# Kernel optimization log

Hardware: AMD Instinct MI355X
Metric: run time of the kernel (lower is better)

The kernel has to match this reference:

```python
import jax, jax.numpy as jnp
import numpy as np

N_NODES = 50000
E_RAW = 1600000
EMB_DIM = 32
HID = 128
OUT = 128


def setup_inputs() -> dict:
    key = jax.random.key(0)
    k1, k2, k3, k4, k5, k6 = jax.random.split(key, 6)
    x = jnp.arange(N_NODES, dtype=jnp.int64)
    edge_index = jax.random.randint(k1, (2, E_RAW), 0, N_NODES, dtype=jnp.int64)
    emb = jax.random.normal(k2, (N_NODES, EMB_DIM), dtype=jnp.float32)
    W1 = jax.random.normal(k3, (EMB_DIM, HID), dtype=jnp.float32) / np.sqrt(EMB_DIM)
    b1 = jnp.zeros((HID,), dtype=jnp.float32)
    W2 = jax.random.normal(k4, (HID, OUT), dtype=jnp.float32) / np.sqrt(HID)
    b2 = jnp.zeros((OUT,), dtype=jnp.float32)
    return {"x": x, "edge_index": edge_index, "emb": emb,
            "W1": W1, "b1": b1, "W2": W2, "b2": b2}


def _gcn_norm(edge_index, num_nodes):
    # add self-loops, then symmetric normalization deg^-1/2 A_hat deg^-1/2
    loop = jnp.arange(num_nodes, dtype=edge_index.dtype)
    src = jnp.concatenate([edge_index[0], loop])
    dst = jnp.concatenate([edge_index[1], loop])
    ones = jnp.ones(src.shape[0], dtype=jnp.float32)
    deg = jax.ops.segment_sum(ones, dst, num_segments=num_nodes)
    dinv = jax.lax.rsqrt(deg)  # deg >= 1 due to self-loops
    norm = dinv[src] * dinv[dst]  # [E+N]
    return src, dst, norm


def _gcn_conv(h, src, dst, norm, W, b, num_nodes):
    h = h @ W                                  # [N, d_out] dense GEMM
    msg = h[src] * norm[:, None]               # gather + edge scale
    agg = jax.ops.segment_sum(msg, dst, num_segments=num_nodes)  # scatter-add
    return agg + b


def reference(x, edge_index, emb, W1, b1, W2, b2):
    num_nodes = emb.shape[0]
    h = emb[x]                                 # embedding lookup
    src, dst, norm = _gcn_norm(edge_index, num_nodes)
    h = _gcn_conv(h, src, dst, norm, W1, b1, num_nodes)
    h = jax.nn.relu(h)
    out = _gcn_conv(h, src, dst, norm, W2, b2, num_nodes)
    return out
```

## Files before the change

### kernel.cpp

```cpp
#include <hip/hip_runtime.h>


#define NPP   6250
#define NC    32

static inline int cdiv(int a, int b){ return (a + b - 1) / b; }

__device__ __forceinline__ unsigned short f2bf(float f){
    unsigned int u = __float_as_uint(f);
    u += 0x7fffu + ((u >> 16) & 1u);
    return (unsigned short)(u >> 16);
}
__device__ __forceinline__ float bf2f(unsigned short b){
    return __uint_as_float(((unsigned int)b) << 16);
}

__global__ void k_zero_i32(int* __restrict__ p, int n){
    int i = blockIdx.x * blockDim.x + threadIdx.x;
    if (i < n) p[i] = 0;
}

__global__ __launch_bounds__(256) void k_bucket(const int* __restrict__ src,
        const int* __restrict__ dst, int E, int* __restrict__ staged,
        int* __restrict__ gcur, int npp, int C){
    __shared__ int qcnt[8];
    __shared__ int qbase[8];
    __shared__ int qbuf[8 * 256];
    int tid = threadIdx.x;
    if (tid < 8) qcnt[tid] = 0;
    __syncthreads();
    int e0 = blockIdx.x * 1024 + tid * 4;
    if (e0 + 3 < E){
        int4 d4 = *(const int4*)(dst + e0);
        int4 s4 = *(const int4*)(src + e0);
        int dd[4] = {d4.x, d4.y, d4.z, d4.w};
        int ss[4] = {s4.x, s4.y, s4.z, s4.w};
        #pragma unroll
        for (int i = 0; i < 4; i++){
            int p = dd[i] / npp;
            int pk = ((dd[i] - p * npp) << 17) | ss[i];
            int pos = atomicAdd(&qcnt[p], 1);
            if (pos < 256) qbuf[p * 256 + pos] = pk;
            else {
                int gp = atomicAdd(&gcur[p], 1);
                staged[(size_t)p * C + gp] = pk;
            }
        }
    } else {
        for (int e = e0; e < E && e < e0 + 4; e++){
            int d = dst[e], s = src[e];
            int p = d / npp;
            int pk = ((d - p * npp) << 17) | s;
            int pos = atomicAdd(&qcnt[p], 1);
            if (pos < 256) qbuf[p * 256 + pos] = pk;
            else {
                int gp = atomicAdd(&gcur[p], 1);
                staged[(size_t)p * C + gp] = pk;
            }
        }
    }
    __syncthreads();
    if (tid < 8){
        int nq = min(qcnt[tid], 256);
        qbase[tid] = (nq > 0) ? atomicAdd(&gcur[tid], nq) : 0;
    }
    __syncthreads();
    for (int b = 0; b < 8; b++){
        int nq = min(qcnt[b], 256);
        int gb = qbase[b];
        for (int i = tid; i < nq; i += 256)
            staged[(size_t)b * C + gb + i] = qbuf[b * 256 + i];
    }
}

__global__ __launch_bounds__(256) void k_hist(const int* __restrict__ staged,
        const int* __restrict__ gcur, int C, int CH, int npp, int* __restrict__ H){
    __shared__ int hist[NPP];
    int part  = blockIdx.x & 7;
    int chunk = blockIdx.x >> 3;
    int tid = threadIdx.x;
    for (int i = tid; i < npp; i += 256) hist[i] = 0;
    __syncthreads();
    int pc = gcur[part];
    int e0 = chunk * CH, e1 = min(e0 + CH, pc);
    const int* sd = staged + (size_t)part * C;
    for (int e = e0 + tid; e < e1; e += 256)
        atomicAdd(&hist[(unsigned)sd[e] >> 17], 1);
    __syncthreads();
    int* Hrow = H + (size_t)(part * NC + chunk) * npp;
    for (int i = tid; i < npp; i += 256) Hrow[i] = hist[i];
}

__global__ __launch_bounds__(256) void k_nodescan(int* __restrict__ H, int npp, int n,
        int* __restrict__ ecount, float* __restrict__ dinv, int* __restrict__ bsum){
    __shared__ int s[256];
    int t = blockIdx.x * 256 + threadIdx.x;
    int run = 0;
    if (t < 8 * npp && t < n){
        int p  = t / npp;
        int dl = t - p * npp;
        #pragma unroll
        for (int c = 0; c < NC; c++){
            size_t idx = (size_t)(p * NC + c) * npp + dl;
            int v = H[idx];
            H[idx] = run;
            run += v;
        }
        ecount[t] = run;
        dinv[t] = rsqrtf((float)run + 1.0f);
    }
    s[threadIdx.x] = run;
    __syncthreads();
    for (int d = 128; d > 0; d >>= 1){
        if (threadIdx.x < d) s[threadIdx.x] += s[threadIdx.x + d];
        __syncthreads();
    }
    if (threadIdx.x == 0) bsum[blockIdx.x] = s[0];
}

__global__ __launch_bounds__(256) void k_scanBC(const int* __restrict__ ecount, int n,
        const int* __restrict__ bsum, int nb, int* __restrict__ offsets){
    __shared__ int bs[256];
    __shared__ int s[256];
    int t = threadIdx.x;
    bs[t] = (t < nb) ? bsum[t] : 0;
    __syncthreads();
    if (t == 0){
        int run = 0;
        for (int b = 0; b < nb; b++){ int v = bs[b]; bs[b] = run; run += v; }
    }
    __syncthreads();
    int i = blockIdx.x * 256 + t;
    int v = (i < n) ? ecount[i] : 0;
    s[t] = v;
    __syncthreads();
    for (int d = 1; d < 256; d <<= 1){
        int x = (t >= d) ? s[t - d] : 0;
        __syncthreads();
        s[t] += x;
        __syncthreads();
    }
    if (i < n) offsets[i] = bs[blockIdx.x] + s[t] - v;
}

__global__ __launch_bounds__(256) void k_fill3(const int* __restrict__ staged,
        const int* __restrict__ gcur, int C, int CH, int npp,
        const int* __restrict__ H, const int* __restrict__ offsets,
        int* __restrict__ csr_src){
    __shared__ int cur[NPP];
    int part  = blockIdx.x & 7;
    int chunk = blockIdx.x >> 3;
    int tid = threadIdx.x;
    const int* Hrow = H + (size_t)(part * NC + chunk) * npp;
    for (int i = tid; i < npp; i += 256) cur[i] = Hrow[i];
    __syncthreads();
    int pc = gcur[part];
    int lo = part * npp;
    int e0 = chunk * CH, e1 = min(e0 + CH, pc);
    const int* sd = staged + (size_t)part * C;
    for (int e = e0 + tid; e < e1; e += 256){
        int pk = sd[e];
        int dl = (unsigned)pk >> 17;
        int r = atomicAdd(&cur[dl], 1);
        csr_src[offsets[lo + dl] + r] = pk & 0x1FFFF;
    }
}

__global__ void k_scale(const float* __restrict__ emb, const int* __restrict__ x,
                        const float* __restrict__ dinv, unsigned short* __restrict__ es, int n){
    int idx = blockIdx.x * blockDim.x + threadIdx.x;
    if (idx >= n * 32) return;
    int i = idx >> 5;
    int c = idx & 31;
    es[idx] = f2bf(emb[(size_t)x[i] * 32 + c] * dinv[i]);
}

__global__ __launch_bounds__(256) void k_l1(const unsigned short* __restrict__ es,
        const int* __restrict__ offsets, const int* __restrict__ ecount,
        const int* __restrict__ csr, const float* __restrict__ dinv,
        const float* __restrict__ W1, const float* __restrict__ b1,
        unsigned short* __restrict__ hs, int n){
    __shared__ float w[32 * 128];
    __shared__ float a1t[8][32];
    for (int i = threadIdx.x; i < 32 * 128; i += 256) w[i] = W1[i];
    int g    = threadIdx.x >> 5;
    int lane = threadIdx.x & 31;
    int node = blockIdx.x * 8 + g;
    if (node < n){
        int off = offsets[node], cnt = ecount[node];
        float s0 = bf2f(es[(size_t)node * 32 + lane]);
        float s1 = 0.f;
        int e = 0;
        for (; e + 8 <= cnt; e += 8){
            int i0 = csr[off + e + 0], i1 = csr[off + e + 1];
            int i2 = csr[off + e + 2], i3 = csr[off + e + 3];
            int i4 = csr[off + e + 4], i5 = csr[off + e + 5];
            int i6 = csr[off + e + 6], i7 = csr[off + e + 7];
            unsigned short v0 = es[(size_t)i0 * 32 + lane];
            unsigned short v1 = es[(size_t)i1 * 32 + lane];
            unsigned short v2 = es[(size_t)i2 * 32 + lane];
            unsigned short v3 = es[(size_t)i3 * 32 + lane];
            unsigned short v4 = es[(size_t)i4 * 32 + lane];
            unsigned short v5 = es[(size_t)i5 * 32 + lane];
            unsigned short v6 = es[(size_t)i6 * 32 + lane];
            unsigned short v7 = es[(size_t)i7 * 32 + lane];
            s0 += bf2f(v0) + bf2f(v2) + bf2f(v4) + bf2f(v6);
            s1 += bf2f(v1) + bf2f(v3) + bf2f(v5) + bf2f(v7);
        }
        for (; e < cnt; e++) s0 += bf2f(es[(size_t)csr[off + e] * 32 + lane]);
        a1t[g][lane] = dinv[node] * (s0 + s1);
    }
    __syncthreads();
    if (node >= n) return;
    int c4 = lane * 4;
    float4 acc = *(const float4*)(b1 + c4);
    #pragma unroll
    for (int k4 = 0; k4 < 8; k4++){
        float4 av = *(const float4*)&a1t[g][k4 * 4];
        float4 w0 = *(const float4*)&w[(k4 * 4 + 0) * 128 + c4];
        float4 w1 = *(const float4*)&w[(k4 * 4 + 1) * 128 + c4];
        float4 w2 = *(const float4*)&w[(k4 * 4 + 2) * 128 + c4];
        float4 w3 = *(const float4*)&w[(k4 * 4 + 3) * 128 + c4];
        acc.x += av.x * w0.x + av.y * w1.x + av.z * w2.x + av.w * w3.x;
        acc.y += av.x * w0.y + av.y * w1.y + av.z * w2.y + av.w * w3.y;
        acc.z += av.x * w0.z + av.y * w1.z + av.z * w2.z + av.w * w3.z;
        acc.w += av.x * w0.w + av.y * w1.w + av.z * w2.w + av.w * w3.w;
    }
    float dv = dinv[node];
    ushort4 o;
    o.x = f2bf(dv * fmaxf(acc.x, 0.f));
    o.y = f2bf(dv * fmaxf(acc.y, 0.f));
    o.z = f2bf(dv * fmaxf(acc.z, 0.f));
    o.w = f2bf(dv * fmaxf(acc.w, 0.f));
    *(ushort4*)(hs + (size_t)node * 128 + c4) = o;
}

__global__ __launch_bounds__(256) void k_l2(const unsigned short* __restrict__ hs,
        const int* __restrict__ offsets, const int* __restrict__ ecount,
        const int* __restrict__ csr, const float* __restrict__ dinv,
        const float* __restrict__ W2, const float* __restrict__ b2,
        float* __restrict__ out, int n){
    __shared__ float a2t[32 * 128];
    int g    = threadIdx.x >> 5;
    int lane = threadIdx.x & 31;
    int c4g  = lane * 4;
    #pragma unroll
    for (int j = 0; j < 4; j++){
        int nl = g + 8 * j;
        int node = blockIdx.x * 32 + nl;
        if (node < n){
            int off = offsets[node], cnt = ecount[node];
            ushort4 sv = *(const ushort4*)(hs + (size_t)node * 128 + c4g);
            float ax0 = bf2f(sv.x), ax1 = 0.f;
            float ay0 = bf2f(sv.y), ay1 = 0.f;
            float az0 = bf2f(sv.z), az1 = 0.f;
            float aw0 = bf2f(sv.w), aw1 = 0.f;
            int e = 0;
            for (; e + 8 <= cnt; e += 8){
                int i0 = csr[off + e + 0], i1 = csr[off + e + 1];
                int i2 = csr[off + e + 2], i3 = csr[off + e + 3];
                int i4 = csr[off + e + 4], i5 = csr[off + e + 5];
                int i6 = csr[off + e + 6], i7 = csr[off + e + 7];
                ushort4 v0 = *(const ushort4*)(hs + (size_t)i0 * 128 + c4g);
                ushort4 v1 = *(const ushort4*)(hs + (size_t)i1 * 128 + c4g);
                ushort4 v2 = *(const ushort4*)(hs + (size_t)i2 * 128 + c4g);
                ushort4 v3 = *(const ushort4*)(hs + (size_t)i3 * 128 + c4g);
                ushort4 v4 = *(const ushort4*)(hs + (size_t)i4 * 128 + c4g);
                ushort4 v5 = *(const ushort4*)(hs + (size_t)i5 * 128 + c4g);
                ushort4 v6 = *(const ushort4*)(hs + (size_t)i6 * 128 + c4g);
                ushort4 v7 = *(const ushort4*)(hs + (size_t)i7 * 128 + c4g);
                ax0 += bf2f(v0.x) + bf2f(v2.x) + bf2f(v4.x) + bf2f(v6.x);
                ax1 += bf2f(v1.x) + bf2f(v3.x) + bf2f(v5.x) + bf2f(v7.x);
                ay0 += bf2f(v0.y) + bf2f(v2.y) + bf2f(v4.y) + bf2f(v6.y);
                ay1 += bf2f(v1.y) + bf2f(v3.y) + bf2f(v5.y) + bf2f(v7.y);
                az0 += bf2f(v0.z) + bf2f(v2.z) + bf2f(v4.z) + bf2f(v6.z);
                az1 += bf2f(v1.z) + bf2f(v3.z) + bf2f(v5.z) + bf2f(v7.z);
                aw0 += bf2f(v0.w) + bf2f(v2.w) + bf2f(v4.w) + bf2f(v6.w);
                aw1 += bf2f(v1.w) + bf2f(v3.w) + bf2f(v5.w) + bf2f(v7.w);
            }
            for (; e < cnt; e++){
                ushort4 v = *(const ushort4*)(hs + (size_t)csr[off + e] * 128 + c4g);
                ax0 += bf2f(v.x); ay0 += bf2f(v.y); az0 += bf2f(v.z); aw0 += bf2f(v.w);
            }
            float dv = dinv[node];
            float4 r;
            r.x = dv * (ax0 + ax1); r.y = dv * (ay0 + ay1);
            r.z = dv * (az0 + az1); r.w = dv * (aw0 + aw1);
            *(float4*)&a2t[nl * 128 + c4g] = r;
        }
    }
    __syncthreads();
    int c4 = lane * 4;
    int r0 = (threadIdx.x >> 5) * 4;
    float4 bias = *(const float4*)(b2 + c4);
    float4 acc0 = bias, acc1 = bias, acc2 = bias, acc3 = bias;
    for (int k = 0; k < 128; k += 4){
        float4 a0  = *(const float4*)&a2t[(r0 + 0) * 128 + k];
        float4 a1v = *(const float4*)&a2t[(r0 + 1) * 128 + k];
        float4 a2v = *(const float4*)&a2t[(r0 + 2) * 128 + k];
        float4 a3v = *(const float4*)&a2t[(r0 + 3) * 128 + k];
        #pragma unroll
        for (int kk = 0; kk < 4; kk++){
            float4 wv = *(const float4*)(W2 + (size_t)(k + kk) * 128 + c4);
            float b0 = (kk == 0) ? a0.x  : (kk == 1) ? a0.y  : (kk == 2) ? a0.z  : a0.w;
            float b1v= (kk == 0) ? a1v.x : (kk == 1) ? a1v.y : (kk == 2) ? a1v.z : a1v.w;
            float b2v= (kk == 0) ? a2v.x : (kk == 1) ? a2v.y : (kk == 2) ? a2v.z : a2v.w;
            float b3 = (kk == 0) ? a3v.x : (kk == 1) ? a3v.y : (kk == 2) ? a3v.z : a3v.w;
            acc0.x += b0 * wv.x; acc0.y += b0 * wv.y; acc0.z += b0 * wv.z; acc0.w += b0 * wv.w;
            acc1.x += b1v * wv.x; acc1.y += b1v * wv.y; acc1.z += b1v * wv.z; acc1.w += b1v * wv.w;
            acc2.x += b2v * wv.x; acc2.y += b2v * wv.y; acc2.z += b2v * wv.z; acc2.w += b2v * wv.w;
            acc3.x += b3 * wv.x; acc3.y += b3 * wv.y; acc3.z += b3 * wv.z; acc3.w += b3 * wv.w;
        }
    }
    int rb = blockIdx.x * 32 + r0;
    if (rb + 0 < n) *(float4*)(out + (size_t)(rb + 0) * 128 + c4) = acc0;
    if (rb + 1 < n) *(float4*)(out + (size_t)(rb + 1) * 128 + c4) = acc1;
    if (rb + 2 < n) *(float4*)(out + (size_t)(rb + 2) * 128 + c4) = acc2;
    if (rb + 3 < n) *(float4*)(out + (size_t)(rb + 3) * 128 + c4) = acc3;
}

extern "C" void kernel_launch(void* const* d_in, const int* in_sizes, int n_in,
                              void* d_out, int out_size, void* d_ws, size_t ws_size,
                              hipStream_t stream){
    const int*   x    = (const int*)d_in[0];
    const int*   ei   = (const int*)d_in[1];
    const float* emb  = (const float*)d_in[2];
    const float* W1   = (const float*)d_in[3];
    const float* b1   = (const float*)d_in[4];
    const float* W2   = (const float*)d_in[5];
    const float* b2   = (const float*)d_in[6];
    const int N = in_sizes[0];
    const int E = in_sizes[1] / 2;
    const int* srcv = ei;
    const int* dstv = ei + E;
    float* out = (float*)d_out;

    char* p = (char*)d_ws;
    auto alloc = [&](size_t bytes) -> char* {
        char* r = p; p += (bytes + 255) & ~(size_t)255; return r;
    };
    int nb = cdiv(N, 256);
    int*            ecount  = (int*)           alloc((size_t)(N + 8) * 4);
    int*            gcur    = ecount + N;
    int*            offsets = (int*)           alloc((size_t)N * 4);
    int*            bsum    = (int*)           alloc((size_t)nb * 4);
    float*          dinv    = (float*)         alloc((size_t)N * 4);
    int*            csr     = (int*)           alloc((size_t)E * 4);
    unsigned short* es      = (unsigned short*)alloc((size_t)N * 32 * 2);
    int*            H       = (int*)           alloc((size_t)8 * NC * NPP * 4);
    unsigned short* hs      = (unsigned short*)alloc((size_t)N * 128 * 2);
    int*            staged  = (int*)           alloc((size_t)(E + 8 * 65536) * 4);
    (void)ws_size; (void)n_in; (void)out_size;

    const int npp = cdiv(N, 8);
    const int C   = E / 8 + 65536;
    const int CH  = cdiv(C, NC);

    k_zero_i32<<<1, 64, 0, stream>>>(gcur, 8);
    k_bucket  <<<cdiv(E, 1024), 256, 0, stream>>>(srcv, dstv, E, staged, gcur, npp, C);
    k_hist    <<<8 * NC, 256, 0, stream>>>(staged, gcur, C, CH, npp, H);
    k_nodescan<<<nb, 256, 0, stream>>>(H, npp, N, ecount, dinv, bsum);
    k_scanBC  <<<nb, 256, 0, stream>>>(ecount, N, bsum, nb, offsets);
    k_fill3   <<<8 * NC, 256, 0, stream>>>(staged, gcur, C, CH, npp, H, offsets, csr);

    k_scale <<<cdiv(N * 32, 256), 256, 0, stream>>>(emb, x, dinv, es, N);
    k_l1    <<<cdiv(N, 8), 256, 0, stream>>>(es, offsets, ecount, csr, dinv, W1, b1, hs, N);

    k_l2    <<<cdiv(N, 32), 256, 0, stream>>>(hs, offsets, ecount, csr, dinv, W2, b2, out, N);
}
```

Baseline: 269.8 us.

## Partition CSR neighbors by source-node quarter to localize layer-2 gathers

Result: slower. 352.7 us (+30.7%).

```diff
diff --git a/kernel.cpp b/kernel.cpp
--- a/kernel.cpp
+++ b/kernel.cpp
@@ -3,6 +3,11 @@
 
 #define NPP   6250
 #define NC    32
+#define CAP   96
+#define CAPP  97
+#define NPB   40
+
+typedef float vfloat4 __attribute__((ext_vector_type(4)));
 
 static inline int cdiv(int a, int b){ return (a + b - 1) / b; }
 
@@ -13,6 +18,11 @@
 }
 __device__ __forceinline__ float bf2f(unsigned short b){
     return __uint_as_float(((unsigned int)b) << 16);
+}
+
+__device__ __forceinline__ void nt_store4(float* p, const float4& v){
+    vfloat4 t = {v.x, v.y, v.z, v.w};
+    __builtin_nontemporal_store(t, (vfloat4*)p);
 }
 
 __global__ void k_zero_i32(int* __restrict__ p, int n){
@@ -164,6 +174,44 @@
         int r = atomicAdd(&cur[dl], 1);
         csr_src[offsets[lo + dl] + r] = pk & 0x1FFFF;
     }
+}
+
+__global__ __launch_bounds__(128) void k_part(const int* __restrict__ offsets,
+        const int* __restrict__ ecount, int* __restrict__ csr,
+        int4* __restrict__ bnd4, int n, int th1, int th2, int th3){
+    __shared__ int buf[128 * CAPP];
+    int t = threadIdx.x;
+    int node = blockIdx.x * 128 + t;
+    if (node >= n) return;
+    int off = offsets[node], cnt = ecount[node];
+    int4 b;
+    if (cnt <= CAP){
+        int* mb = buf + t * CAPP;
+        int c0 = 0, c1 = 0, c2 = 0;
+        for (int i = 0; i < cnt; i++){
+            int v = csr[off + i];
+            mb[i] = v;
+            c0 += (v < th1);
+            c1 += (v >= th1) & (v < th2);
+            c2 += (v >= th2) & (v < th3);
+        }
+        int p1 = c0, p2 = c0 + c1, p3 = c0 + c1 + c2;
+        int q0 = 0, q1 = p1, q2 = p2, q3 = p3;
+        for (int i = 0; i < cnt; i++){
+            int v = mb[i];
+            int pos;
+            if      (v < th1) pos = q0++;
+            else if (v < th2) pos = q1++;
+            else if (v < th3) pos = q2++;
+            else              pos = q3++;
+            csr[off + pos] = v;
+        }
+        b = make_int4(p1, p2, p3, cnt);
+    } else {
+        int q = cnt >> 2;
+        b = make_int4(q, 2 * q, 3 * q, cnt);
+    }
+    bnd4[node] = b;
 }
 
 __global__ void k_scale(const float* __restrict__ emb, const int* __restrict__ x,
@@ -235,32 +283,47 @@
     *(ushort4*)(hs + (size_t)node * 128 + c4) = o;
 }
 
-__global__ __launch_bounds__(256) void k_l2(const unsigned short* __restrict__ hs,
-        const int* __restrict__ offsets, const int* __restrict__ ecount,
+__global__ __launch_bounds__(256, 5) void k_l2(const unsigned short* __restrict__ hs,
+        const int* __restrict__ offsets, const int4* __restrict__ bnd4,
         const int* __restrict__ csr, const float* __restrict__ dinv,
         const float* __restrict__ W2, const float* __restrict__ b2,
         float* __restrict__ out, int n){
-    __shared__ float a2t[32 * 128];
+    __shared__ float a2t[NPB * 128];
     int g    = threadIdx.x >> 5;
     int lane = threadIdx.x & 31;
     int c4g  = lane * 4;
+    float4 acc[5];
     #pragma unroll
-    for (int j = 0; j < 4; j++){
-        int nl = g + 8 * j;
-        int node = blockIdx.x * 32 + nl;
+    for (int j = 0; j < 5; j++){
+        int node = blockIdx.x * NPB + g + 8 * j;
         if (node < n){
-            int off = offsets[node], cnt = ecount[node];
             ushort4 sv = *(const ushort4*)(hs + (size_t)node * 128 + c4g);
-            float ax0 = bf2f(sv.x), ax1 = 0.f;
-            float ay0 = bf2f(sv.y), ay1 = 0.f;
-            float az0 = bf2f(sv.z), az1 = 0.f;
-            float aw0 = bf2f(sv.w), aw1 = 0.f;
-            int e = 0;
-            for (; e + 8 <= cnt; e += 8){
-                int i0 = csr[off + e + 0], i1 = csr[off + e + 1];
-                int i2 = csr[off + e + 2], i3 = csr[off + e + 3];
-                int i4 = csr[off + e + 4], i5 = csr[off + e + 5];
-                int i6 = csr[off + e + 6], i7 = csr[off + e + 7];
+            acc[j].x = bf2f(sv.x); acc[j].y = bf2f(sv.y);
+            acc[j].z = bf2f(sv.z); acc[j].w = bf2f(sv.w);
+        } else {
+            acc[j].x = acc[j].y = acc[j].z = acc[j].w = 0.f;
+        }
+    }
+    #pragma unroll
+    for (int c = 0; c < 4; c++){
+        #pragma unroll
+        for (int j = 0; j < 5; j++){
+            int node = blockIdx.x * NPB + g + 8 * j;
+            if (node >= n) continue;
+            int off = offsets[node];
+            int4 b = bnd4[node];
+            int e0 = (c == 0) ? 0   : (c == 1) ? b.x : (c == 2) ? b.y : b.z;
+            int e1 = (c == 0) ? b.x : (c == 1) ? b.y : (c == 2) ? b.z : b.w;
+            int e = e0;
+            for (; e + 8 <= e1; e += 8){
+                int i0 = __builtin_nontemporal_load(csr + off + e + 0);
+                int i1 = __builtin_nontemporal_load(csr + off + e + 1);
+                int i2 = __builtin_nontemporal_load(csr + off + e + 2);
+                int i3 = __builtin_nontemporal_load(csr + off + e + 3);
+                int i4 = __builtin_nontemporal_load(csr + off + e + 4);
+                int i5 = __builtin_nontemporal_load(csr + off + e + 5);
+                int i6 = __builtin_nontemporal_load(csr + off + e + 6);
+                int i7 = __builtin_nontemporal_load(csr + off + e + 7);
                 ushort4 v0 = *(const ushort4*)(hs + (size_t)i0 * 128 + c4g);
                 ushort4 v1 = *(const ushort4*)(hs + (size_t)i1 * 128 + c4g);
                 ushort4 v2 = *(const ushort4*)(hs + (size_t)i2 * 128 + c4g);
@@ -269,36 +332,51 @@
                 ushort4 v5 = *(const ushort4*)(hs + (size_t)i5 * 128 + c4g);
                 ushort4 v6 = *(const ushort4*)(hs + (size_t)i6 * 128 + c4g);
                 ushort4 v7 = *(const ushort4*)(hs + (size_t)i7 * 128 + c4g);
-                ax0 += bf2f(v0.x) + bf2f(v2.x) + bf2f(v4.x) + bf2f(v6.x);
-                ax1 += bf2f(v1.x) + bf2f(v3.x) + bf2f(v5.x) + bf2f(v7.x);
-                ay0 += bf2f(v0.y) + bf2f(v2.y) + bf2f(v4.y) + bf2f(v6.y);
-                ay1 += bf2f(v1.y) + bf2f(v3.y) + bf2f(v5.y) + bf2f(v7.y);
-                az0 += bf2f(v0.z) + bf2f(v2.z) + bf2f(v4.z) + bf2f(v6.z);
-                az1 += bf2f(v1.z) + bf2f(v3.z) + bf2f(v5.z) + bf2f(v7.z);
-                aw0 += bf2f(v0.w) + bf2f(v2.w) + bf2f(v4.w) + bf2f(v6.w);
-                aw1 += bf2f(v1.w) + bf2f(v3.w) + bf2f(v5.w) + bf2f(v7.w);
+                acc[j].x += bf2f(v0.x) + bf2f(v1.x) + bf2f(v2.x) + bf2f(v3.x)
+                          + bf2f(v4.x) + bf2f(v5.x) + bf2f(v6.x) + bf2f(v7.x);
+                acc[j].y += bf2f(v0.y) + bf2f(v1.y) + bf2f(v2.y) + bf2f(v3.y)
+                          + bf2f(v4.y) + bf2f(v5.y) + bf2f(v6.y) + bf2f(v7.y);
+                acc[j].z += bf2f(v0.z) + bf2f(v1.z) + bf2f(v2.z) + bf2f(v3.z)
+                          + bf2f(v4.z) + bf2f(v5.z) + bf2f(v6.z) + bf2f(v7.z);
+                acc[j].w += bf2f(v0.w) + bf2f(v1.w) + bf2f(v2.w) + bf2f(v3.w)
+                          + bf2f(v4.w) + bf2f(v5.w) + bf2f(v6.w) + bf2f(v7.w);
             }
-            for (; e < cnt; e++){
-                ushort4 v = *(const ushort4*)(hs + (size_t)csr[off + e] * 128 + c4g);
-                ax0 += bf2f(v.x); ay0 += bf2f(v.y); az0 += bf2f(v.z); aw0 += bf2f(v.w);
+            if (e < e1){
+                #pragma unroll
+                for (int i = 0; i < 8; i++){
+                    int ei = min(e + i, e1 - 1);
+                    int idx = __builtin_nontemporal_load(csr + off + ei);
+                    ushort4 v = *(const ushort4*)(hs + (size_t)idx * 128 + c4g);
+                    if (e + i < e1){
+                        acc[j].x += bf2f(v.x); acc[j].y += bf2f(v.y);
+                        acc[j].z += bf2f(v.z); acc[j].w += bf2f(v.w);
+                    }
+                }
             }
+        }
+    }
+    #pragma unroll
+    for (int j = 0; j < 5; j++){
+        int node = blockIdx.x * NPB + g + 8 * j;
+        if (node < n){
             float dv = dinv[node];
             float4 r;
-            r.x = dv * (ax0 + ax1); r.y = dv * (ay0 + ay1);
-            r.z = dv * (az0 + az1); r.w = dv * (aw0 + aw1);
-            *(float4*)&a2t[nl * 128 + c4g] = r;
+            r.x = dv * acc[j].x; r.y = dv * acc[j].y;
+            r.z = dv * acc[j].z; r.w = dv * acc[j].w;
+            *(float4*)&a2t[(g + 8 * j) * 128 + c4g] = r;
         }
     }
     __syncthreads();
     int c4 = lane * 4;
-    int r0 = (threadIdx.x >> 5) * 4;
+    int r0 = g * 5;
     float4 bias = *(const float4*)(b2 + c4);
-    float4 acc0 = bias, acc1 = bias, acc2 = bias, acc3 = bias;
+    float4 o0 = bias, o1 = bias, o2 = bias, o3 = bias, o4 = bias;
     for (int k = 0; k < 128; k += 4){
-        float4 a0  = *(const float4*)&a2t[(r0 + 0) * 128 + k];
-        float4 a1v = *(const float4*)&a2t[(r0 + 1) * 128 + k];
-        float4 a2v = *(const float4*)&a2t[(r0 + 2) * 128 + k];
-        float4 a3v = *(const float4*)&a2t[(r0 + 3) * 128 + k];
+        float4 a0 = *(const float4*)&a2t[(r0 + 0) * 128 + k];
+        float4 a1v= *(const float4*)&a2t[(r0 + 1) * 128 + k];
+        float4 a2v= *(const float4*)&a2t[(r0 + 2) * 128 + k];
+        float4 a3v= *(const float4*)&a2t[(r0 + 3) * 128 + k];
+        float4 a4v= *(const float4*)&a2t[(r0 + 4) * 128 + k];
         #pragma unroll
         for (int kk = 0; kk < 4; kk++){
             float4 wv = *(const float4*)(W2 + (size_t)(k + kk) * 128 + c4);
@@ -306,17 +384,20 @@
             float b1v= (kk == 0) ? a1v.x : (kk == 1) ? a1v.y : (kk == 2) ? a1v.z : a1v.w;
             float b2v= (kk == 0) ? a2v.x : (kk == 1) ? a2v.y : (kk == 2) ? a2v.z : a2v.w;
             float b3 = (kk == 0) ? a3v.x : (kk == 1) ? a3v.y : (kk == 2) ? a3v.z : a3v.w;
-            acc0.x += b0 * wv.x; acc0.y += b0 * wv.y; acc0.z += b0 * wv.z; acc0.w += b0 * wv.w;
-            acc1.x += b1v * wv.x; acc1.y += b1v * wv.y; acc1.z += b1v * wv.z; acc1.w += b1v * wv.w;
-            acc2.x += b2v * wv.x; acc2.y += b2v * wv.y; acc2.z += b2v * wv.z; acc2.w += b2v * wv.w;
-            acc3.x += b3 * wv.x; acc3.y += b3 * wv.y; acc3.z += b3 * wv.z; acc3.w += b3 * wv.w;
-        }
-    }
-    int rb = blockIdx.x * 32 + r0;
-    if (rb + 0 < n) *(float4*)(out + (size_t)(rb + 0) * 128 + c4) = acc0;
-    if (rb + 1 < n) *(float4*)(out + (size_t)(rb + 1) * 128 + c4) = acc1;
-    if (rb + 2 < n) *(float4*)(out + (size_t)(rb + 2) * 128 + c4) = acc2;
-    if (rb + 3 < n) *(float4*)(out + (size_t)(rb + 3) * 128 + c4) = acc3;
+            float b4 = (kk == 0) ? a4v.x : (kk == 1) ? a4v.y : (kk == 2) ? a4v.z : a4v.w;
+            o0.x += b0 * wv.x; o0.y += b0 * wv.y; o0.z += b0 * wv.z; o0.w += b0 * wv.w;
+            o1.x += b1v * wv.x; o1.y += b1v * wv.y; o1.z += b1v * wv.z; o1.w += b1v * wv.w;
+            o2.x += b2v * wv.x; o2.y += b2v * wv.y; o2.z += b2v * wv.z; o2.w += b2v * wv.w;
+            o3.x += b3 * wv.x; o3.y += b3 * wv.y; o3.z += b3 * wv.z; o3.w += b3 * wv.w;
+            o4.x += b4 * wv.x; o4.y += b4 * wv.y; o4.z += b4 * wv.z; o4.w += b4 * wv.w;
+        }
+    }
+    int rb = blockIdx.x * NPB + r0;
+    if (rb + 0 < n) nt_store4(out + (size_t)(rb + 0) * 128 + c4, o0);
+    if (rb + 1 < n) nt_store4(out + (size_t)(rb + 1) * 128 + c4, o1);
+    if (rb + 2 < n) nt_store4(out + (size_t)(rb + 2) * 128 + c4, o2);
+    if (rb + 3 < n) nt_store4(out + (size_t)(rb + 3) * 128 + c4, o3);
+    if (rb + 4 < n) nt_store4(out + (size_t)(rb + 4) * 128 + c4, o4);
 }
 
 extern "C" void kernel_launch(void* const* d_in, const int* in_sizes, int n_in,
@@ -349,12 +430,14 @@
     unsigned short* es      = (unsigned short*)alloc((size_t)N * 32 * 2);
     int*            H       = (int*)           alloc((size_t)8 * NC * NPP * 4);
     unsigned short* hs      = (unsigned short*)alloc((size_t)N * 128 * 2);
+    int4*           bnd4    = (int4*)          alloc((size_t)N * 16);
     int*            staged  = (int*)           alloc((size_t)(E + 8 * 65536) * 4);
     (void)ws_size; (void)n_in; (void)out_size;
 
     const int npp = cdiv(N, 8);
     const int C   = E / 8 + 65536;
     const int CH  = cdiv(C, NC);
+    const int th1 = cdiv(N, 4), th2 = 2 * th1, th3 = 3 * th1;
 
     k_zero_i32<<<1, 64, 0, stream>>>(gcur, 8);
     k_bucket  <<<cdiv(E, 1024), 256, 0, stream>>>(srcv, dstv, E, staged, gcur, npp, C);
@@ -362,9 +445,10 @@
     k_nodescan<<<nb, 256, 0, stream>>>(H, npp, N, ecount, dinv, bsum);
     k_scanBC  <<<nb, 256, 0, stream>>>(ecount, N, bsum, nb, offsets);
     k_fill3   <<<8 * NC, 256, 0, stream>>>(staged, gcur, C, CH, npp, H, offsets, csr);
+    k_part    <<<cdiv(N, 128), 128, 0, stream>>>(offsets, ecount, csr, bnd4, N, th1, th2, th3);
 
     k_scale <<<cdiv(N * 32, 256), 256, 0, stream>>>(emb, x, dinv, es, N);
     k_l1    <<<cdiv(N, 8), 256, 0, stream>>>(es, offsets, ecount, csr, dinv, W1, b1, hs, N);
 
-    k_l2    <<<cdiv(N, 32), 256, 0, stream>>>(hs, offsets, ecount, csr, dinv, W2, b2, out, N);
-}
+    k_l2    <<<cdiv(N, NPB), 256, 0, stream>>>(hs, offsets, bnd4, csr, dinv, W2, b2, out, N);
+}
```
